# Optimization experiments

Hardware: AMD Instinct MI355X
Metric: run time of the kernel (lower is better)

## Reference

```python
import jax, jax.numpy as jnp
import numpy as np

D_MODEL = 768
NUM_HEADS = 12
D_HEAD = D_MODEL // NUM_HEADS


def setup_inputs() -> dict:
    key = jax.random.key(0)
    ks = jax.random.split(key, 12)
    B, S = 2, 2048
    s = 1.0 / np.sqrt(D_MODEL)
    inp = {
        "query": jax.random.normal(ks[0], (B, S, D_MODEL), dtype=jnp.float32),
        "key": jax.random.normal(ks[1], (B, S, D_MODEL), dtype=jnp.float32),
        "value": jax.random.normal(ks[2], (B, S, D_MODEL), dtype=jnp.float32),
        "mask": jax.random.randint(ks[3], (B, 1, 1, S), 0, 2, dtype=jnp.int32),
        "Wq": jax.random.normal(ks[4], (D_MODEL, D_MODEL), dtype=jnp.float32) * s,
        "bq": jnp.zeros((D_MODEL,), dtype=jnp.float32),
        "Wk": jax.random.normal(ks[5], (D_MODEL, D_MODEL), dtype=jnp.float32) * s,
        "bk": jnp.zeros((D_MODEL,), dtype=jnp.float32),
        "Wv": jax.random.normal(ks[6], (D_MODEL, D_MODEL), dtype=jnp.float32) * s,
        "bv": jnp.zeros((D_MODEL,), dtype=jnp.float32),
        "Wo": jax.random.normal(ks[7], (D_MODEL, D_MODEL), dtype=jnp.float32) * s,
        "bo": jnp.zeros((D_MODEL,), dtype=jnp.float32),
    }
    return inp


def _split_heads(x):
    # [B, S, D] -> [B, H, S, Dh]
    B, S, _ = x.shape
    return x.reshape(B, S, NUM_HEADS, D_HEAD).transpose(0, 2, 1, 3)


def reference(query, key, value, mask, Wq, bq, Wk, bk, Wv, bv, Wo, bo):
    q = _split_heads(query @ Wq + bq)
    k = _split_heads(key @ Wk + bk)
    v = _split_heads(value @ Wv + bv)
    scores = jnp.einsum("bhqd,bhkd->bhqk", q, k) / jnp.sqrt(jnp.float32(D_HEAD))
    scores = jnp.where(mask == 0, -jnp.inf, scores)
    attn = jax.nn.softmax(scores, axis=-1)  # dropout is identity at inference
    ctx = jnp.einsum("bhqk,bhkd->bhqd", attn, v)
    B, _, S, _ = ctx.shape
    ctx = ctx.transpose(0, 2, 1, 3).reshape(B, S, D_MODEL)
    return ctx @ Wo + bo
```

## Files before the change

kernel.cpp:

```cpp
#include <hip/hip_runtime.h>
#include <stdint.h>

#define D_MODEL 768
#define SEQ     2048
#define BATCH   2
#define NHEAD   12
#define DHEAD   64
#define MROWS   (BATCH * SEQ)

typedef __bf16 bf16x8 __attribute__((ext_vector_type(8)));
typedef float  f32x4  __attribute__((ext_vector_type(4)));
typedef unsigned short u16;
typedef u16 u16x4 __attribute__((ext_vector_type(4)));
typedef uint32_t u32;

__device__ __forceinline__ u16 f32_to_bf16(float x) {
    u32 u = __float_as_uint(x);
    u32 r = (u + 0x7FFFu + ((u >> 16) & 1u)) >> 16;
    return (u16)r;
}
__device__ __forceinline__ float bf16_to_f32(u16 h) {
    return __uint_as_float(((u32)h) << 16);
}
__device__ __forceinline__ void split2(float x, u16 &hi, u16 &lo) {
    hi = f32_to_bf16(x);
    lo = f32_to_bf16(x - bf16_to_f32(hi));
}
__device__ __forceinline__ u32 pack2(float a, float b) {
    return ((u32)f32_to_bf16(b) << 16) | (u32)f32_to_bf16(a);
}

__device__ __forceinline__ void stage16(const u16* g, const u16* l) {
    __builtin_amdgcn_global_load_lds(
        (const __attribute__((address_space(1))) u32*)g,
        (__attribute__((address_space(3))) u32*)l,
        16, 0, 0);
}

#define QSCALE 0.1803368801111204f
#define MSHIFT 20.0f

__global__ void prep_split_x(const float* __restrict__ q, const float* __restrict__ k,
                             const float* __restrict__ v, u16* __restrict__ xbase)
{
    const int t = blockIdx.y;
    const float* src = (t == 0) ? q : (t == 1) ? k : v;
    const size_t P = (size_t)MROWS * D_MODEL;
    u16* xh = xbase + (size_t)t * 2 * P;
    u16* xl = xh + P;
    size_t idx = ((size_t)blockIdx.x * 256 + threadIdx.x) * 4;
    float4 val = *reinterpret_cast<const float4*>(&src[idx]);
    float vv[4] = {val.x, val.y, val.z, val.w};
    u16x4 h4, l4;
    #pragma unroll
    for (int j = 0; j < 4; ++j) { u16 h, l; split2(vv[j], h, l); h4[j] = h; l4[j] = l; }
    *reinterpret_cast<u16x4*>(&xh[idx]) = h4;
    *reinterpret_cast<u16x4*>(&xl[idx]) = l4;
}

__global__ void prep_wt(const float* __restrict__ Wq, const float* __restrict__ Wk,
                        const float* __restrict__ Wv, const float* __restrict__ Wo,
                        u16* __restrict__ wtbase)
{
    const int w = blockIdx.z;
    const float* W = (w == 0) ? Wq : (w == 1) ? Wk : (w == 2) ? Wv : Wo;
    const size_t WP = (size_t)D_MODEL * D_MODEL;
    u16* th = wtbase + (size_t)w * 2 * WP;
    u16* tl = th + WP;

    __shared__ float tile[32][33];
    const int tx = threadIdx.x & 31, ty = threadIdx.x >> 5;
    const int n0 = blockIdx.x * 32, k0 = blockIdx.y * 32;
    #pragma unroll
    for (int r = 0; r < 4; ++r) {
        int kk = k0 + ty + r * 8;
        tile[ty + r * 8][tx] = W[(size_t)kk * D_MODEL + n0 + tx];
    }
    __syncthreads();
    #pragma unroll
    for (int r = 0; r < 4; ++r) {
        int n = n0 + ty + r * 8;
        float v = tile[tx][ty + r * 8];
        u16 h, l; split2(v, h, l);
        th[(size_t)n * D_MODEL + k0 + tx] = h;
        tl[(size_t)n * D_MODEL + k0 + tx] = l;
    }
}

__global__ void prep_bias(const int* __restrict__ Mask, float* __restrict__ BiasM)
{
    int i = blockIdx.x * 256 + threadIdx.x;
    BiasM[i] = (Mask[i] == 0) ? -3e38f : -MSHIFT;
}

__global__ __launch_bounds__(256, 4) void gemm3(
    const u16* __restrict__ Ah0, const u16* __restrict__ Al0,
    const u16* __restrict__ Ah1, const u16* __restrict__ Al1,
    const u16* __restrict__ Ah2, const u16* __restrict__ Al2,
    const u16* __restrict__ Bh0, const u16* __restrict__ Bl0,
    const u16* __restrict__ Bh1, const u16* __restrict__ Bl1,
    const u16* __restrict__ Bh2, const u16* __restrict__ Bl2,
    const float* __restrict__ bias0, const float* __restrict__ bias1,
    const float* __restrict__ bias2,
    u16* __restrict__ Qhl, u16* __restrict__ Khl, u16* __restrict__ Vt,
    float* __restrict__ Out, int mode)
{
    const int z = (mode == 3) ? 3 : (int)blockIdx.z;
    const u16 *GAh, *GAl, *GBh, *GBl; const float* Bias;
    if (z == 1)      { GAh = Ah1; GAl = Al1; GBh = Bh1; GBl = Bl1; Bias = bias1; }
    else if (z == 2) { GAh = Ah2; GAl = Al2; GBh = Bh2; GBl = Bl2; Bias = bias2; }
    else             { GAh = Ah0; GAl = Al0; GBh = Bh0; GBl = Bl0; Bias = bias0; }

    const int m0 = blockIdx.x * 128;
    const int n0 = blockIdx.y * 64;
    const int tid  = threadIdx.x;
    const int wave = tid >> 6, lane = tid & 63;
    const int quad = lane >> 4, l16 = lane & 15;
    const int wm = wave & 1, wn = wave >> 1;

    __shared__ u16 sAh[128 * 32];
    __shared__ u16 sAl[128 * 32];
    __shared__ u16 sBh[64 * 32];
    __shared__ u16 sBl[64 * 32];

    const int srow = lane >> 2;
    const int sc8  = (lane & 3) * 8;

    f32x4 acc[4][2] = {};

    for (int k0 = 0; k0 < D_MODEL; k0 += 32) {
        {
            #pragma unroll
            for (int i = 0; i < 2; ++i) {
                int row = wave * 32 + i * 16 + srow;
                size_t ga = (size_t)(m0 + row) * D_MODEL + k0 + sc8;
                int ldst = (wave * 32 + i * 16) * 32;
                stage16(&GAh[ga], &sAh[ldst]);
                stage16(&GAl[ga], &sAl[ldst]);
            }
            int row = wave * 16 + srow;
            size_t gb = (size_t)(n0 + row) * D_MODEL + k0 + sc8;
            int ldst = (wave * 16) * 32;
            stage16(&GBh[gb], &sBh[ldst]);
            stage16(&GBl[gb], &sBl[ldst]);
        }
        asm volatile("s_waitcnt vmcnt(0)" ::: "memory");
        __syncthreads();

        bf16x8 afh[4], afl[4], bfh[2], bfl[2];
        #pragma unroll
        for (int t = 0; t < 4; ++t) {
            int ar = wm * 64 + t * 16 + l16;
            afh[t] = *reinterpret_cast<const bf16x8*>(&sAh[ar * 32 + quad * 8]);
            afl[t] = *reinterpret_cast<const bf16x8*>(&sAl[ar * 32 + quad * 8]);
        }
        #pragma unroll
        for (int t = 0; t < 2; ++t) {
            int bc = wn * 32 + t * 16 + l16;
            bfh[t] = *reinterpret_cast<const bf16x8*>(&sBh[bc * 32 + quad * 8]);
            bfl[t] = *reinterpret_cast<const bf16x8*>(&sBl[bc * 32 + quad * 8]);
        }
        #pragma unroll
        for (int mt = 0; mt < 4; ++mt) {
            #pragma unroll
            for (int nt = 0; nt < 2; ++nt) {
                f32x4 a = acc[mt][nt];
                a = __builtin_amdgcn_mfma_f32_16x16x32_bf16(afh[mt], bfh[nt], a, 0, 0, 0);
                a = __builtin_amdgcn_mfma_f32_16x16x32_bf16(afh[mt], bfl[nt], a, 0, 0, 0);
                a = __builtin_amdgcn_mfma_f32_16x16x32_bf16(afl[mt], bfh[nt], a, 0, 0, 0);
                acc[mt][nt] = a;
            }
        }
        __syncthreads();
    }

    #pragma unroll
    for (int nt = 0; nt < 2; ++nt) {
        int n = n0 + wn * 32 + nt * 16 + l16;
        float bv = Bias[n];
        #pragma unroll
        for (int mt = 0; mt < 4; ++mt) {
            #pragma unroll
            for (int r = 0; r < 4; ++r) {
                int m = m0 + wm * 64 + mt * 16 + quad * 4 + r;
                float v = acc[mt][nt][r] + bv;
                if (mode == 3) {
                    Out[(size_t)m * D_MODEL + n] = v;
                } else {
                    int b = m >> 11, s = m & (SEQ - 1);
                    int h = n >> 6, d = n & 63;
                    size_t bh = (size_t)(b * NHEAD + h);
                    if (z == 0) {
                        u16 hi, lo; split2(v * QSCALE, hi, lo);
                        u16* base = &Qhl[(bh * SEQ + s) * 128];
                        base[d] = hi; base[d + 64] = lo;
                    } else if (z == 1) {
                        u16 hi, lo; split2(v, hi, lo);
                        u16* base = &Khl[(bh * SEQ + s) * 128];
                        base[d] = hi; base[d + 64] = lo;
                    } else {
                        Vt[(bh * DHEAD + d) * SEQ + s] = f32_to_bf16(v);
                    }
                }
            }
        }
    }
}

__global__ __launch_bounds__(256, 3) void attn_kernel(
    const u16* __restrict__ Qhl, const u16* __restrict__ Khl, const u16* __restrict__ Vt,
    const float* __restrict__ BiasM, float* __restrict__ Opart,
    float* __restrict__ Lpart)
{
    const int qt   = blockIdx.x;
    const int bh   = blockIdx.y;
    const int half = blockIdx.z;
    const int b    = bh / NHEAD;
    const int tid  = threadIdx.x;
    const int wave = tid >> 6, lane = tid & 63;
    const int quad = lane >> 4, l16 = lane & 15;

    __shared__ u16 sK[4 * 2048];
    __shared__ u16 sV[2 * 2048];

    bf16x8 qh0[2], qh1[2], ql0[2], ql1[2];
    #pragma unroll
    for (int g = 0; g < 2; ++g) {
        const u16* qbase = &Qhl[((size_t)bh * SEQ + qt * 128 + wave * 32 + g * 16 + l16) * 128];
        qh0[g] = *reinterpret_cast<const bf16x8*>(&qbase[quad * 8]);
        qh1[g] = *reinterpret_cast<const bf16x8*>(&qbase[32 + quad * 8]);
        ql0[g] = *reinterpret_cast<const bf16x8*>(&qbase[64 + quad * 8]);
        ql1[g] = *reinterpret_cast<const bf16x8*>(&qbase[96 + quad * 8]);
    }

    float lrow[2] = {0.f, 0.f};
    f32x4 oacc[2][4] = {};

    const float* biasb = &BiasM[b * SEQ];
    const int srcl0 = (((quad * 2) & 3) << 4) | l16;
    const int srcl1 = (((quad * 2 + 1) & 3) << 4) | l16;
    const bool selhi = (quad >> 1) != 0;

    const int strow = wave * 16 + (lane >> 2);
    const int stc8  = (lane & 3) * 8;
    const u16* kgb = &Khl[(size_t)bh * SEQ * 128];
    const u16* vgb = &Vt[(size_t)bh * DHEAD * SEQ];

    const int kvbeg = half * (SEQ / 2);
    for (int kv0 = kvbeg; kv0 < kvbeg + SEQ / 2; kv0 += 64) {
        #pragma unroll
        for (int j = 0; j < 4; ++j)
            stage16(&kgb[(size_t)(kv0 + strow) * 128 + j * 32 + stc8],
                    &sK[j * 2048 + wave * 512]);
        #pragma unroll
        for (int j = 0; j < 2; ++j)
            stage16(&vgb[(size_t)strow * SEQ + kv0 + j * 32 + stc8],
                    &sV[j * 2048 + wave * 512]);
        asm volatile("s_waitcnt vmcnt(0)" ::: "memory");
        __syncthreads();

        f32x4 binit[4];
        #pragma unroll
        for (int mt = 0; mt < 4; ++mt) {
            float4 b4 = *reinterpret_cast<const float4*>(
                &biasb[kv0 + mt * 16 + quad * 4]);
            binit[mt][0] = b4.x; binit[mt][1] = b4.y;
            binit[mt][2] = b4.z; binit[mt][3] = b4.w;
        }

        #pragma unroll
        for (int g = 0; g < 2; ++g) {
            f32x4 sacc[4];
            #pragma unroll
            for (int mt = 0; mt < 4; ++mt) {
                const int rb = (mt * 16 + l16) * 32 + quad * 8;
                bf16x8 kh0 = *reinterpret_cast<const bf16x8*>(&sK[rb]);
                bf16x8 kh1 = *reinterpret_cast<const bf16x8*>(&sK[2048 + rb]);
                bf16x8 kl0 = *reinterpret_cast<const bf16x8*>(&sK[4096 + rb]);
                bf16x8 kl1 = *reinterpret_cast<const bf16x8*>(&sK[6144 + rb]);
                f32x4 s = binit[mt];
                s = __builtin_amdgcn_mfma_f32_16x16x32_bf16(kh0, qh0[g], s, 0, 0, 0);
                s = __builtin_amdgcn_mfma_f32_16x16x32_bf16(kh1, qh1[g], s, 0, 0, 0);
                s = __builtin_amdgcn_mfma_f32_16x16x32_bf16(kh0, ql0[g], s, 0, 0, 0);
                s = __builtin_amdgcn_mfma_f32_16x16x32_bf16(kh1, ql1[g], s, 0, 0, 0);
                s = __builtin_amdgcn_mfma_f32_16x16x32_bf16(kl0, qh0[g], s, 0, 0, 0);
                s = __builtin_amdgcn_mfma_f32_16x16x32_bf16(kl1, qh1[g], s, 0, 0, 0);
                sacc[mt] = s;
            }

            u32 pLo[4], pHi[4];
            #pragma unroll
            for (int mt = 0; mt < 4; ++mt) {
                float p0 = exp2f(sacc[mt][0]);
                float p1 = exp2f(sacc[mt][1]);
                float p2 = exp2f(sacc[mt][2]);
                float p3 = exp2f(sacc[mt][3]);
                lrow[g] += (p0 + p1) + (p2 + p3);
                pLo[mt] = pack2(p0, p1);
                pHi[mt] = pack2(p2, p3);
            }

            union FU { u32 u[4]; bf16x8 v; } fr[2];
            #pragma unroll
            for (int f = 0; f < 2; ++f) {
                u32 a, bb;
                a  = (u32)__shfl((int)pLo[2 * f],     srcl0, 64);
                bb = (u32)__shfl((int)pLo[2 * f + 1], srcl0, 64);
                fr[f].u[0] = selhi ? bb : a;
                a  = (u32)__shfl((int)pHi[2 * f],     srcl0, 64);
                bb = (u32)__shfl((int)pHi[2 * f + 1], srcl0, 64);
                fr[f].u[1] = selhi ? bb : a;
                a  = (u32)__shfl((int)pLo[2 * f],     srcl1, 64);
                bb = (u32)__shfl((int)pLo[2 * f + 1], srcl1, 64);
                fr[f].u[2] = selhi ? bb : a;
                a  = (u32)__shfl((int)pHi[2 * f],     srcl1, 64);
                bb = (u32)__shfl((int)pHi[2 * f + 1], srcl1, 64);
                fr[f].u[3] = selhi ? bb : a;
            }

            #pragma unroll
            for (int dt = 0; dt < 4; ++dt) {
                const int rb = (dt * 16 + l16) * 32 + quad * 8;
                bf16x8 vb0 = *reinterpret_cast<const bf16x8*>(&sV[rb]);
                bf16x8 vb1 = *reinterpret_cast<const bf16x8*>(&sV[2048 + rb]);
                oacc[g][dt] = __builtin_amdgcn_mfma_f32_16x16x32_bf16(vb0, fr[0].v, oacc[g][dt], 0, 0, 0);
                oacc[g][dt] = __builtin_amdgcn_mfma_f32_16x16x32_bf16(vb1, fr[1].v, oacc[g][dt], 0, 0, 0);
            }
        }
        __syncthreads();
    }

    #pragma unroll
    for (int g = 0; g < 2; ++g) {
        float l = lrow[g];
        l += __shfl_xor(l, 16, 64);
        l += __shfl_xor(l, 32, 64);
        size_t rowb = ((size_t)(half * (BATCH * NHEAD) + bh)) * SEQ
                    + qt * 128 + wave * 32 + g * 16 + l16;
        float* ob = &Opart[rowb * 64];
        #pragma unroll
        for (int dt = 0; dt < 4; ++dt)
            *reinterpret_cast<f32x4*>(&ob[dt * 16 + quad * 4]) = oacc[g][dt];
        if (quad == 0) Lpart[rowb] = l;
    }
}

__global__ void attn_combine(const float* __restrict__ Opart,
                             const float* __restrict__ Lpart,
                             u16* __restrict__ CTXh, u16* __restrict__ CTXl)
{
    const int NROW = BATCH * NHEAD * SEQ;
    int t = blockIdx.x * 256 + threadIdx.x;
    int row = t >> 4;
    int d0 = (t & 15) << 2;
    float inv = 1.f / (Lpart[row] + Lpart[NROW + row]);
    f32x4 O0 = *reinterpret_cast<const f32x4*>(&Opart[(size_t)row * 64 + d0]);
    f32x4 O1 = *reinterpret_cast<const f32x4*>(&Opart[((size_t)NROW + row) * 64 + d0]);
    int bh = row >> 11, q = row & (SEQ - 1);
    int b = bh / NHEAD, h = bh % NHEAD;
    size_t off = ((size_t)(b * SEQ + q)) * D_MODEL + h * DHEAD + d0;
    u16x4 h4, l4;
    #pragma unroll
    for (int j = 0; j < 4; ++j) {
        float val = (O0[j] + O1[j]) * inv;
        u16 hi, lo; split2(val, hi, lo);
        h4[j] = hi; l4[j] = lo;
    }
    *reinterpret_cast<u16x4*>(&CTXh[off]) = h4;
    *reinterpret_cast<u16x4*>(&CTXl[off]) = l4;
}

extern "C" void kernel_launch(void* const* d_in, const int* in_sizes, int n_in,
                              void* d_out, int out_size, void* d_ws, size_t ws_size,
                              hipStream_t stream)
{
    const float* query = (const float*)d_in[0];
    const float* key   = (const float*)d_in[1];
    const float* value = (const float*)d_in[2];
    const int*   mask  = (const int*)d_in[3];
    const float* Wq = (const float*)d_in[4];
    const float* bq = (const float*)d_in[5];
    const float* Wk = (const float*)d_in[6];
    const float* bk = (const float*)d_in[7];
    const float* Wv = (const float*)d_in[8];
    const float* bv = (const float*)d_in[9];
    const float* Wo = (const float*)d_in[10];
    const float* bo = (const float*)d_in[11];

    char* ws = (char*)d_ws;
    const size_t P2  = (size_t)MROWS * D_MODEL * 2;
    const size_t WP2 = (size_t)D_MODEL * D_MODEL * 2;

    u16* Xbase = (u16*)ws;
    u16* Xh_q = Xbase;                       u16* Xl_q = (u16*)((char*)Xh_q + P2);
    u16* Xh_k = (u16*)((char*)Xbase + 2*P2); u16* Xl_k = (u16*)((char*)Xh_k + P2);
    u16* Xh_v = (u16*)((char*)Xbase + 4*P2); u16* Xl_v = (u16*)((char*)Xh_v + P2);

    char* wtb = ws + 6 * P2;
    u16* Wh_q = (u16*)wtb;                   u16* Wl_q = (u16*)(wtb + WP2);
    u16* Wh_k = (u16*)(wtb + 2*WP2);         u16* Wl_k = (u16*)(wtb + 3*WP2);
    u16* Wh_v = (u16*)(wtb + 4*WP2);         u16* Wl_v = (u16*)(wtb + 5*WP2);
    u16* Wh_o = (u16*)(wtb + 6*WP2);         u16* Wl_o = (u16*)(wtb + 7*WP2);

    char* qb = wtb + 8 * WP2;
    const size_t QK_BYTES = (size_t)BATCH * NHEAD * SEQ * 128 * 2;
    u16* QhlBuf = (u16*)qb;
    u16* KhlBuf = (u16*)(qb + QK_BYTES);
    u16* VtBuf  = (u16*)(qb + 2 * QK_BYTES);

    char* tail = qb + 2 * QK_BYTES + QK_BYTES / 2;
    float* BiasM = (float*)tail;
    float* Lpart = (float*)(tail + 16384);

    float* Opart = (float*)Xh_k;
    u16* CTXh = Xh_q; u16* CTXl = Xl_q;

    float* out = (float*)d_out;
    dim3 blk(256, 1, 1);

    prep_split_x<<<dim3(3072, 3), blk, 0, stream>>>(query, key, value, Xbase);
    prep_wt<<<dim3(24, 24, 4), blk, 0, stream>>>(Wq, Wk, Wv, Wo, (u16*)wtb);
    prep_bias<<<dim3(16), blk, 0, stream>>>(mask, BiasM);

    gemm3<<<dim3(32, 12, 3), blk, 0, stream>>>(
        Xh_q, Xl_q, Xh_k, Xl_k, Xh_v, Xl_v,
        Wh_q, Wl_q, Wh_k, Wl_k, Wh_v, Wl_v,
        bq, bk, bv, QhlBuf, KhlBuf, VtBuf, nullptr, 0);

    attn_kernel<<<dim3(16, 24, 2), blk, 0, stream>>>(
        QhlBuf, KhlBuf, VtBuf, BiasM, Opart, Lpart);

    attn_combine<<<dim3(3072), blk, 0, stream>>>(Opart, Lpart, CTXh, CTXl);

    gemm3<<<dim3(32, 12, 1), blk, 0, stream>>>(
        CTXh, CTXl, nullptr, nullptr, nullptr, nullptr,
        Wh_o, Wl_o, nullptr, nullptr, nullptr, nullptr,
        bo, nullptr, nullptr, nullptr, nullptr, nullptr, out, 3);
}
```

Baseline: 281.9 us.

## Fuse prep kernels, compute softmax row sums via MFMA, truncate P packing, reorder attention loops

```diff
diff --git a/kernel.cpp b/kernel.cpp
--- a/kernel.cpp
+++ b/kernel.cpp
@@ -26,8 +26,8 @@
     hi = f32_to_bf16(x);
     lo = f32_to_bf16(x - bf16_to_f32(hi));
 }
-__device__ __forceinline__ u32 pack2(float a, float b) {
-    return ((u32)f32_to_bf16(b) << 16) | (u32)f32_to_bf16(a);
+__device__ __forceinline__ u32 pack2t(float a, float b) {
+    return __builtin_amdgcn_perm(__float_as_uint(b), __float_as_uint(a), 0x07060302u);
 }
 
 __device__ __forceinline__ void stage16(const u16* g, const u16* l) {
@@ -40,57 +40,57 @@
 #define QSCALE 0.1803368801111204f
 #define MSHIFT 20.0f
 
-__global__ void prep_split_x(const float* __restrict__ q, const float* __restrict__ k,
-                             const float* __restrict__ v, u16* __restrict__ xbase)
+__global__ void prep_all(const float* __restrict__ q, const float* __restrict__ k,
+                         const float* __restrict__ v, u16* __restrict__ xbase,
+                         const float* __restrict__ Wq, const float* __restrict__ Wk,
+                         const float* __restrict__ Wv, const float* __restrict__ Wo,
+                         u16* __restrict__ wtbase,
+                         const int* __restrict__ Mask, float* __restrict__ BiasM)
 {
-    const int t = blockIdx.y;
-    const float* src = (t == 0) ? q : (t == 1) ? k : v;
-    const size_t P = (size_t)MROWS * D_MODEL;
-    u16* xh = xbase + (size_t)t * 2 * P;
-    u16* xl = xh + P;
-    size_t idx = ((size_t)blockIdx.x * 256 + threadIdx.x) * 4;
-    float4 val = *reinterpret_cast<const float4*>(&src[idx]);
-    float vv[4] = {val.x, val.y, val.z, val.w};
-    u16x4 h4, l4;
-    #pragma unroll
-    for (int j = 0; j < 4; ++j) { u16 h, l; split2(vv[j], h, l); h4[j] = h; l4[j] = l; }
-    *reinterpret_cast<u16x4*>(&xh[idx]) = h4;
-    *reinterpret_cast<u16x4*>(&xl[idx]) = l4;
-}
-
-__global__ void prep_wt(const float* __restrict__ Wq, const float* __restrict__ Wk,
-                        const float* __restrict__ Wv, const float* __restrict__ Wo,
-                        u16* __restrict__ wtbase)
-{
-    const int w = blockIdx.z;
-    const float* W = (w == 0) ? Wq : (w == 1) ? Wk : (w == 2) ? Wv : Wo;
-    const size_t WP = (size_t)D_MODEL * D_MODEL;
-    u16* th = wtbase + (size_t)w * 2 * WP;
-    u16* tl = th + WP;
-
     __shared__ float tile[32][33];
-    const int tx = threadIdx.x & 31, ty = threadIdx.x >> 5;
-    const int n0 = blockIdx.x * 32, k0 = blockIdx.y * 32;
-    #pragma unroll
-    for (int r = 0; r < 4; ++r) {
-        int kk = k0 + ty + r * 8;
-        tile[ty + r * 8][tx] = W[(size_t)kk * D_MODEL + n0 + tx];
-    }
-    __syncthreads();
-    #pragma unroll
-    for (int r = 0; r < 4; ++r) {
-        int n = n0 + ty + r * 8;
-        float v = tile[tx][ty + r * 8];
-        u16 h, l; split2(v, h, l);
-        th[(size_t)n * D_MODEL + k0 + tx] = h;
-        tl[(size_t)n * D_MODEL + k0 + tx] = l;
-    }
-}
-
-__global__ void prep_bias(const int* __restrict__ Mask, float* __restrict__ BiasM)
-{
-    int i = blockIdx.x * 256 + threadIdx.x;
-    BiasM[i] = (Mask[i] == 0) ? -3e38f : -MSHIFT;
+    const int bx = blockIdx.x;
+    if (bx < 9216) {
+        const int t = bx / 3072;
+        const float* src = (t == 0) ? q : (t == 1) ? k : v;
+        const size_t P = (size_t)MROWS * D_MODEL;
+        u16* xh = xbase + (size_t)t * 2 * P;
+        u16* xl = xh + P;
+        size_t idx = ((size_t)(bx % 3072) * 256 + threadIdx.x) * 4;
+        float4 val = *reinterpret_cast<const float4*>(&src[idx]);
+        float vv[4] = {val.x, val.y, val.z, val.w};
+        u16x4 h4, l4;
+        #pragma unroll
+        for (int j = 0; j < 4; ++j) { u16 h, l; split2(vv[j], h, l); h4[j] = h; l4[j] = l; }
+        *reinterpret_cast<u16x4*>(&xh[idx]) = h4;
+        *reinterpret_cast<u16x4*>(&xl[idx]) = l4;
+    } else if (bx < 11520) {
+        int r = bx - 9216;
+        int w = r / 576; r %= 576;
+        int ky = r / 24, nx = r % 24;
+        const float* W = (w == 0) ? Wq : (w == 1) ? Wk : (w == 2) ? Wv : Wo;
+        const size_t WP = (size_t)D_MODEL * D_MODEL;
+        u16* th = wtbase + (size_t)w * 2 * WP;
+        u16* tl = th + WP;
+        const int tx = threadIdx.x & 31, ty = threadIdx.x >> 5;
+        const int n0 = nx * 32, k0 = ky * 32;
+        #pragma unroll
+        for (int rr = 0; rr < 4; ++rr) {
+            int kk = k0 + ty + rr * 8;
+            tile[ty + rr * 8][tx] = W[(size_t)kk * D_MODEL + n0 + tx];
+        }
+        __syncthreads();
+        #pragma unroll
+        for (int rr = 0; rr < 4; ++rr) {
+            int n = n0 + ty + rr * 8;
+            float val = tile[tx][ty + rr * 8];
+            u16 h, l; split2(val, h, l);
+            th[(size_t)n * D_MODEL + k0 + tx] = h;
+            tl[(size_t)n * D_MODEL + k0 + tx] = l;
+        }
+    } else {
+        int i = (bx - 11520) * 256 + threadIdx.x;
+        BiasM[i] = (Mask[i] == 0) ? -3e38f : -MSHIFT;
+    }
 }
 
 __global__ __launch_bounds__(256, 4) void gemm3(
@@ -233,8 +233,13 @@
         ql1[g] = *reinterpret_cast<const bf16x8*>(&qbase[96 + quad * 8]);
     }
 
-    float lrow[2] = {0.f, 0.f};
+    union OU { u16 u[8]; bf16x8 v; } onesu;
+    #pragma unroll
+    for (int j = 0; j < 8; ++j) onesu.u[j] = 0x3F80;
+    const bf16x8 ones = onesu.v;
+
     f32x4 oacc[2][4] = {};
+    f32x4 lacc[2] = {};
 
     const float* biasb = &BiasM[b * SEQ];
     const int srcl0 = (((quad * 2) & 3) << 4) | l16;
@@ -268,16 +273,16 @@
             binit[mt][2] = b4.z; binit[mt][3] = b4.w;
         }
 
-        #pragma unroll
-        for (int g = 0; g < 2; ++g) {
-            f32x4 sacc[4];
-            #pragma unroll
-            for (int mt = 0; mt < 4; ++mt) {
-                const int rb = (mt * 16 + l16) * 32 + quad * 8;
-                bf16x8 kh0 = *reinterpret_cast<const bf16x8*>(&sK[rb]);
-                bf16x8 kh1 = *reinterpret_cast<const bf16x8*>(&sK[2048 + rb]);
-                bf16x8 kl0 = *reinterpret_cast<const bf16x8*>(&sK[4096 + rb]);
-                bf16x8 kl1 = *reinterpret_cast<const bf16x8*>(&sK[6144 + rb]);
+        f32x4 sacc[2][4];
+        #pragma unroll
+        for (int mt = 0; mt < 4; ++mt) {
+            const int rb = (mt * 16 + l16) * 32 + quad * 8;
+            bf16x8 kh0 = *reinterpret_cast<const bf16x8*>(&sK[rb]);
+            bf16x8 kh1 = *reinterpret_cast<const bf16x8*>(&sK[2048 + rb]);
+            bf16x8 kl0 = *reinterpret_cast<const bf16x8*>(&sK[4096 + rb]);
+            bf16x8 kl1 = *reinterpret_cast<const bf16x8*>(&sK[6144 + rb]);
+            #pragma unroll
+            for (int g = 0; g < 2; ++g) {
                 f32x4 s = binit[mt];
                 s = __builtin_amdgcn_mfma_f32_16x16x32_bf16(kh0, qh0[g], s, 0, 0, 0);
                 s = __builtin_amdgcn_mfma_f32_16x16x32_bf16(kh1, qh1[g], s, 0, 0, 0);
@@ -285,63 +290,69 @@
                 s = __builtin_amdgcn_mfma_f32_16x16x32_bf16(kh1, ql1[g], s, 0, 0, 0);
                 s = __builtin_amdgcn_mfma_f32_16x16x32_bf16(kl0, qh0[g], s, 0, 0, 0);
                 s = __builtin_amdgcn_mfma_f32_16x16x32_bf16(kl1, qh1[g], s, 0, 0, 0);
-                sacc[mt] = s;
-            }
-
+                sacc[g][mt] = s;
+            }
+        }
+
+        union FU { u32 u[4]; bf16x8 v; } fr[2][2];
+        #pragma unroll
+        for (int g = 0; g < 2; ++g) {
             u32 pLo[4], pHi[4];
             #pragma unroll
             for (int mt = 0; mt < 4; ++mt) {
-                float p0 = exp2f(sacc[mt][0]);
-                float p1 = exp2f(sacc[mt][1]);
-                float p2 = exp2f(sacc[mt][2]);
-                float p3 = exp2f(sacc[mt][3]);
-                lrow[g] += (p0 + p1) + (p2 + p3);
-                pLo[mt] = pack2(p0, p1);
-                pHi[mt] = pack2(p2, p3);
-            }
-
-            union FU { u32 u[4]; bf16x8 v; } fr[2];
+                float p0 = exp2f(sacc[g][mt][0]);
+                float p1 = exp2f(sacc[g][mt][1]);
+                float p2 = exp2f(sacc[g][mt][2]);
+                float p3 = exp2f(sacc[g][mt][3]);
+                pLo[mt] = pack2t(p0, p1);
+                pHi[mt] = pack2t(p2, p3);
+            }
             #pragma unroll
             for (int f = 0; f < 2; ++f) {
                 u32 a, bb;
                 a  = (u32)__shfl((int)pLo[2 * f],     srcl0, 64);
                 bb = (u32)__shfl((int)pLo[2 * f + 1], srcl0, 64);
-                fr[f].u[0] = selhi ? bb : a;
+                fr[g][f].u[0] = selhi ? bb : a;
                 a  = (u32)__shfl((int)pHi[2 * f],     srcl0, 64);
                 bb = (u32)__shfl((int)pHi[2 * f + 1], srcl0, 64);
-                fr[f].u[1] = selhi ? bb : a;
+                fr[g][f].u[1] = selhi ? bb : a;
                 a  = (u32)__shfl((int)pLo[2 * f],     srcl1, 64);
                 bb = (u32)__shfl((int)pLo[2 * f + 1], srcl1, 64);
-                fr[f].u[2] = selhi ? bb : a;
+                fr[g][f].u[2] = selhi ? bb : a;
                 a  = (u32)__shfl((int)pHi[2 * f],     srcl1, 64);
                 bb = (u32)__shfl((int)pHi[2 * f + 1], srcl1, 64);
-                fr[f].u[3] = selhi ? bb : a;
-            }
-
-            #pragma unroll
-            for (int dt = 0; dt < 4; ++dt) {
-                const int rb = (dt * 16 + l16) * 32 + quad * 8;
-                bf16x8 vb0 = *reinterpret_cast<const bf16x8*>(&sV[rb]);
-                bf16x8 vb1 = *reinterpret_cast<const bf16x8*>(&sV[2048 + rb]);
-                oacc[g][dt] = __builtin_amdgcn_mfma_f32_16x16x32_bf16(vb0, fr[0].v, oacc[g][dt], 0, 0, 0);
-                oacc[g][dt] = __builtin_amdgcn_mfma_f32_16x16x32_bf16(vb1, fr[1].v, oacc[g][dt], 0, 0, 0);
-            }
+                fr[g][f].u[3] = selhi ? bb : a;
+            }
+        }
+
+        #pragma unroll
+        for (int dt = 0; dt < 4; ++dt) {
+            const int rb = (dt * 16 + l16) * 32 + quad * 8;
+            bf16x8 vb0 = *reinterpret_cast<const bf16x8*>(&sV[rb]);
+            bf16x8 vb1 = *reinterpret_cast<const bf16x8*>(&sV[2048 + rb]);
+            #pragma unroll
+            for (int g = 0; g < 2; ++g) {
+                oacc[g][dt] = __builtin_amdgcn_mfma_f32_16x16x32_bf16(vb0, fr[g][0].v, oacc[g][dt], 0, 0, 0);
+                oacc[g][dt] = __builtin_amdgcn_mfma_f32_16x16x32_bf16(vb1, fr[g][1].v, oacc[g][dt], 0, 0, 0);
+            }
+        }
+        #pragma unroll
+        for (int g = 0; g < 2; ++g) {
+            lacc[g] = __builtin_amdgcn_mfma_f32_16x16x32_bf16(ones, fr[g][0].v, lacc[g], 0, 0, 0);
+            lacc[g] = __builtin_amdgcn_mfma_f32_16x16x32_bf16(ones, fr[g][1].v, lacc[g], 0, 0, 0);
         }
         __syncthreads();
     }
 
     #pragma unroll
     for (int g = 0; g < 2; ++g) {
-        float l = lrow[g];
-        l += __shfl_xor(l, 16, 64);
-        l += __shfl_xor(l, 32, 64);
         size_t rowb = ((size_t)(half * (BATCH * NHEAD) + bh)) * SEQ
                     + qt * 128 + wave * 32 + g * 16 + l16;
         float* ob = &Opart[rowb * 64];
         #pragma unroll
         for (int dt = 0; dt < 4; ++dt)
             *reinterpret_cast<f32x4*>(&ob[dt * 16 + quad * 4]) = oacc[g][dt];
-        if (quad == 0) Lpart[rowb] = l;
+        if (quad == 0) Lpart[rowb] = lacc[g][0];
     }
 }
 
@@ -418,9 +429,8 @@
     float* out = (float*)d_out;
     dim3 blk(256, 1, 1);
 
-    prep_split_x<<<dim3(3072, 3), blk, 0, stream>>>(query, key, value, Xbase);
-    prep_wt<<<dim3(24, 24, 4), blk, 0, stream>>>(Wq, Wk, Wv, Wo, (u16*)wtb);
-    prep_bias<<<dim3(16), blk, 0, stream>>>(mask, BiasM);
+    prep_all<<<dim3(11536), blk, 0, stream>>>(
+        query, key, value, Xbase, Wq, Wk, Wv, Wo, (u16*)wtb, mask, BiasM);
 
     gemm3<<<dim3(32, 12, 3), blk, 0, stream>>>(
         Xh_q, Xl_q, Xh_k, Xl_k, Xh_v, Xl_v,
```

Result: faster. 269.8 us (-4.3%).
